# Optimization experiments

Hardware: AMD Instinct MI355X
Metric: run time of the kernel (lower is better)

## Reference

```python
import jax, jax.numpy as jnp
import numpy as np
import math

N_HEADS = 16

def _ln(x, g, b, eps=1e-5):
    m = jnp.mean(x, axis=-1, keepdims=True)
    v = jnp.var(x, axis=-1, keepdims=True)
    return (x - m) * jax.lax.rsqrt(v + eps) * g + b

def _block(x, ln1_g, ln1_b, ln2_g, ln2_b, wqkv, wo, w1, w2):
    b, k, d = x.shape
    dh = d // N_HEADS
    h = _ln(x, ln1_g, ln1_b)
    qkv = (h @ wqkv).reshape(b, k, 3, N_HEADS, dh)
    q, kk, v = qkv[:, :, 0], qkv[:, :, 1], qkv[:, :, 2]
    scores = jnp.einsum('bqhd,bkhd->bhqk', q, kk) / math.sqrt(dh)
    attn = jax.nn.softmax(scores, axis=-1)
    o = jnp.einsum('bhqk,bkhd->bqhd', attn, v).reshape(b, k, d) @ wo
    x = x + o
    h2 = _ln(x, ln2_g, ln2_b)
    return x + jax.nn.gelu(h2 @ w1) @ w2

def setup_inputs() -> dict:
    key = jax.random.key(0)
    ks = jax.random.split(key, 6)
    b, s, d, dff = 4, 4096, 1024, 4096
    sc = 0.02
    return {
        'x': jax.random.normal(ks[0], (b, s, d), jnp.float32),
        'router_w': jax.random.normal(ks[1], (d,), jnp.float32) * sc,
        'ln1_g': jnp.ones((d,), jnp.float32),
        'ln1_b': jnp.zeros((d,), jnp.float32),
        'ln2_g': jnp.ones((d,), jnp.float32),
        'ln2_b': jnp.zeros((d,), jnp.float32),
        'wqkv': jax.random.normal(ks[2], (d, 3 * d), jnp.float32) * sc,
        'wo': jax.random.normal(ks[3], (d, d), jnp.float32) * sc,
        'w1': jax.random.normal(ks[4], (d, dff), jnp.float32) * sc,
        'w2': jax.random.normal(ks[5], (dff, d), jnp.float32) * sc,
    }

def reference(x, router_w, ln1_g, ln1_b, ln2_g, ln2_b, wqkv, wo, w1, w2):
    b, s, d = x.shape
    K = s // 2  # top_k = int(s * capacity_factor), capacity_factor = 0.5
    logits = x @ router_w                      # [b, s]
    w, idx = jax.lax.top_k(logits, K)          # [b, K]
    order = jnp.argsort(idx, axis=1)           # sort selected tokens by position
    sel = jnp.take_along_axis(idx, order, axis=1)          # [b, K] sorted indices
    fx = jnp.take_along_axis(x, sel[..., None], axis=1)    # gather routed tokens [b, K, d]
    xo = _block(fx, ln1_g, ln1_b, ln2_g, ln2_b, wqkv, wo, w1, w2)
    rw = jnp.take_along_axis(jax.nn.softmax(w, axis=1), order, axis=1)[..., None]  # [b, K, 1]
    batch_idx = jnp.arange(b)[:, None]
    out = x.at[batch_idx, sel].add(rw * xo)    # softmax-weighted scatter-add
    return out
```

## Files before the change

### kernel.cpp

```cpp
#include <hip/hip_runtime.h>
#include <hip/hip_bf16.h>
#include <stdint.h>

typedef __hip_bfloat16 bf16;
typedef __attribute__((ext_vector_type(8))) short short8;
typedef __attribute__((ext_vector_type(4))) float f32x4;
typedef __attribute__((ext_vector_type(2))) unsigned uint2v;
typedef __attribute__((ext_vector_type(4))) unsigned uint4v;
typedef __attribute__((ext_vector_type(4))) unsigned short ushort4v;

#define B_   4
#define S_   4096
#define D_   1024
#define KSEL 2048
#define DFF  4096
#define NH   16
#define DH   64

static __device__ __forceinline__ void load_lds16(const void* g, void* l) {
  __builtin_amdgcn_global_load_lds((const __attribute__((address_space(1))) void*)g,
                                   (__attribute__((address_space(3))) void*)l,
                                   16, 0, 0);
}

static __device__ __forceinline__ short8 scale8(short8 v, float s) {
  short8 r;
#pragma unroll
  for (int i = 0; i < 8; ++i) {
    unsigned u = ((unsigned)(unsigned short)v[i]) << 16;
    float f = __uint_as_float(u) * s;
    bf16 o = __float2bfloat16(f);
    short t;
    __builtin_memcpy(&t, &o, 2);
    r[i] = t;
  }
  return r;
}

static __device__ __forceinline__ unsigned cvt_pk_bf16(float lo, float hi) {
  unsigned r;
  asm("v_cvt_pk_bf16_f32 %0, %1, %2" : "=v"(r) : "v"(lo), "v"(hi));
  return r;
}

static __device__ __forceinline__ void pl32_swap(unsigned &a, unsigned &b) {
#if __has_builtin(__builtin_amdgcn_permlane32_swap)
  uint2v r = __builtin_amdgcn_permlane32_swap(a, b, false, false);
  a = r[0]; b = r[1];
#else
  asm("v_permlane32_swap_b32 %0, %1" : "+v"(a), "+v"(b));
#endif
}

static __device__ __forceinline__ void pl16_swap(unsigned &a, unsigned &b) {
#if __has_builtin(__builtin_amdgcn_permlane16_swap)
  uint2v r = __builtin_amdgcn_permlane16_swap(a, b, false, false);
  a = r[0]; b = r[1];
#else
  asm("v_permlane16_swap_b32 %0, %1" : "+v"(a), "+v"(b));
#endif
}

__global__ __launch_bounds__(256)
void copy_router(const float* __restrict__ x, const float* __restrict__ rwts,
                 float* __restrict__ out, float* __restrict__ logits)
{
  int s = blockIdx.x, b = blockIdx.y;
  int tid = threadIdx.x;
  const float4* row = (const float4*)(x + ((size_t)b * S_ + s) * D_);
  float4 v = row[tid];
  ((float4*)(out + ((size_t)b * S_ + s) * D_))[tid] = v;
  float4 rv = ((const float4*)rwts)[tid];
  float p = v.x * rv.x + v.y * rv.y + v.z * rv.z + v.w * rv.w;
  for (int off = 32; off; off >>= 1) p += __shfl_down(p, off, 64);
  __shared__ float wsum[4];
  if ((tid & 63) == 0) wsum[tid >> 6] = p;
  __syncthreads();
  if (tid == 0) logits[(size_t)b * S_ + s] = wsum[0] + wsum[1] + wsum[2] + wsum[3];
}

__global__ __launch_bounds__(1024)
void topk_kernel(const float* __restrict__ logits,
                 int* __restrict__ sel, float* __restrict__ rw)
{
  __shared__ float lg[4096];
  __shared__ unsigned long long keys[4096];
  __shared__ unsigned char flags[4096];
  __shared__ float wsum[16];
  __shared__ int wtot[16];
  __shared__ int woff[17];

  int b = blockIdx.x, tid = threadIdx.x;
  const float* L = logits + (size_t)b * S_;
  for (int i = tid; i < 4096; i += 1024) {
    float v = L[i];
    lg[i] = v;
    unsigned u = __float_as_uint(v);
    u = (u & 0x80000000u) ? ~u : (u | 0x80000000u);
    u = ~u;
    keys[i] = ((unsigned long long)u << 32) | (unsigned)i;
  }
  __syncthreads();
  for (int k = 2; k <= 4096; k <<= 1) {
    for (int j = k >> 1; j > 0; j >>= 1) {
      for (int t = tid; t < 4096; t += 1024) {
        int ixj = t ^ j;
        if (ixj > t) {
          bool up = ((t & k) == 0);
          unsigned long long a = keys[t], c = keys[ixj];
          if ((a > c) == up) { keys[t] = c; keys[ixj] = a; }
        }
      }
      __syncthreads();
    }
  }
  for (int i = tid; i < 4096; i += 1024) flags[i] = 0;
  __syncthreads();
  for (int i = tid; i < KSEL; i += 1024) flags[(int)(keys[i] & 0xFFFFFFFFu)] = 1;
  __syncthreads();
  float m = lg[(int)(keys[0] & 0xFFFFFFFFu)];
  float part = 0.f;
  for (int i = tid; i < KSEL; i += 1024) part += __expf(lg[(int)(keys[i] & 0xFFFFFFFFu)] - m);
  for (int off = 32; off; off >>= 1) part += __shfl_down(part, off, 64);
  if ((tid & 63) == 0) wsum[tid >> 6] = part;
  __syncthreads();
  if (tid == 0) { float t = 0; for (int w = 0; w < 16; ++w) t += wsum[w]; wsum[0] = t; }
  __syncthreads();
  float inv = 1.0f / wsum[0];
  int base = tid * 4;
  int f0 = flags[base], f1 = flags[base + 1], f2 = flags[base + 2], f3 = flags[base + 3];
  int mysum = f0 + f1 + f2 + f3;
  int incl = mysum;
  int lane = tid & 63;
  for (int off = 1; off < 64; off <<= 1) {
    int t = __shfl_up(incl, off, 64);
    if (lane >= off) incl += t;
  }
  if (lane == 63) wtot[tid >> 6] = incl;
  __syncthreads();
  if (tid == 0) { int sacc = 0; for (int w = 0; w < 16; ++w) { woff[w] = sacc; sacc += wtot[w]; } woff[16] = sacc; }
  __syncthreads();
  int p = woff[tid >> 6] + incl - mysum;
  int fl[4] = { f0, f1, f2, f3 };
  for (int q = 0; q < 4; ++q) {
    if (fl[q]) {
      int idx = base + q;
      sel[b * KSEL + p] = idx;
      rw[b * KSEL + p] = __expf(lg[idx] - m) * inv;
      p++;
    }
  }
}

__global__ __launch_bounds__(256)
void ln_kernel(const float* __restrict__ in, const float* __restrict__ x,
               const int* __restrict__ sel,
               const float* __restrict__ g, const float* __restrict__ beta,
               bf16* __restrict__ out, int gather)
{
  int r = blockIdx.x;
  int tid = threadIdx.x;
  const float* src;
  if (gather) {
    int b = r >> 11, t = r & 2047;
    src = x + ((size_t)b * S_ + sel[b * KSEL + t]) * D_;
  } else {
    src = in + (size_t)r * D_;
  }
  float4 v = ((const float4*)src)[tid];
  float s = v.x + v.y + v.z + v.w;
  float sq = v.x * v.x + v.y * v.y + v.z * v.z + v.w * v.w;
  for (int off = 32; off; off >>= 1) { s += __shfl_down(s, off, 64); sq += __shfl_down(sq, off, 64); }
  __shared__ float wsA[4], wsB[4];
  if ((tid & 63) == 0) { wsA[tid >> 6] = s; wsB[tid >> 6] = sq; }
  __syncthreads();
  float stot = wsA[0] + wsA[1] + wsA[2] + wsA[3];
  float sqt  = wsB[0] + wsB[1] + wsB[2] + wsB[3];
  float mean = stot * (1.f / 1024.f);
  float var  = sqt * (1.f / 1024.f) - mean * mean;
  float rs = rsqrtf(var + 1e-5f);
  float4 gv = ((const float4*)g)[tid];
  float4 bv = ((const float4*)beta)[tid];
  bf16* o = out + (size_t)r * D_ + tid * 4;
  o[0] = __float2bfloat16((v.x - mean) * rs * gv.x + bv.x);
  o[1] = __float2bfloat16((v.y - mean) * rs * gv.y + bv.y);
  o[2] = __float2bfloat16((v.z - mean) * rs * gv.z + bv.z);
  o[3] = __float2bfloat16((v.w - mean) * rs * gv.w + bv.w);
}

__global__ __launch_bounds__(256)
void wtrans(const float* __restrict__ in, bf16* __restrict__ out, int K, int N)
{
  __shared__ float tile[32][33];
  int n0 = blockIdx.x * 32, k0 = blockIdx.y * 32;
  int r = threadIdx.x >> 5, c = threadIdx.x & 31;
#pragma unroll
  for (int i = 0; i < 4; ++i)
    tile[r + 8 * i][c] = in[(size_t)(k0 + r + 8 * i) * N + n0 + c];
  __syncthreads();
#pragma unroll
  for (int i = 0; i < 4; ++i)
    out[(size_t)(n0 + r + 8 * i) * K + k0 + c] = __float2bfloat16(tile[c][r + 8 * i]);
}

__global__ __launch_bounds__(256)
void vt_transpose(const bf16* __restrict__ qkv, bf16* __restrict__ vt)
{
  __shared__ bf16 tile[32][33];
  int bh = blockIdx.z;
  int d0 = blockIdx.y * 32;
  int t0 = blockIdx.x * 32;
  int b = bh >> 4, h = bh & 15;
  int r = threadIdx.x >> 5, c = threadIdx.x & 31;
#pragma unroll
  for (int i = 0; i < 4; ++i) {
    int t = t0 + r + 8 * i;
    tile[r + 8 * i][c] = qkv[(size_t)(b * KSEL + t) * 3072 + 2048 + h * 64 + d0 + c];
  }
  __syncthreads();
#pragma unroll
  for (int i = 0; i < 4; ++i) {
    int d = d0 + r + 8 * i;
    vt[((size_t)bh * 64 + d) * KSEL + t0 + c] = tile[c][r + 8 * i];
  }
}

template<int EPI, int TN>
__global__ __launch_bounds__(256)
void gemm_bt(const bf16* __restrict__ A, const bf16* __restrict__ Bt,
             float* __restrict__ Cf, bf16* __restrict__ Cb,
             int M, int N, int K,
             const float* __restrict__ xin, const int* __restrict__ sel,
             const float* __restrict__ rw, const float* __restrict__ x1,
             float* __restrict__ outp)
{
  constexpr int NT = TN / 32;
  constexpr int WN = TN / 2;
  __shared__ bf16 As[128 * 64];
  __shared__ bf16 Bs[TN * 64];
  const int tid = threadIdx.x;
  const int wid = tid >> 6;
  const int lane = tid & 63;
  const int l15 = lane & 15;
  const int quad = lane >> 4;
  const int wm = wid >> 1, wn = wid & 1;
  const int bm = blockIdx.x * 128;
  const int bn = blockIdx.y * TN;

  const int srow = lane >> 3;
  const int sgrp = (lane & 7) ^ srow;

  f32x4 acc[4][NT] = {};

  for (int k0 = 0; k0 < K; k0 += 64) {
#pragma unroll
    for (int c2 = 0; c2 < 4; ++c2) {
      int c = wid * 4 + c2;
      const bf16* ga = A + (size_t)(bm + c * 8 + srow) * K + (k0 + sgrp * 8);
      load_lds16(ga, &As[c * 512]);
    }
#pragma unroll
    for (int c2 = 0; c2 < TN / 32; ++c2) {
      int c = wid * (TN / 32) + c2;
      const bf16* gb = Bt + (size_t)(bn + c * 8 + srow) * K + (k0 + sgrp * 8);
      load_lds16(gb, &Bs[c * 512]);
    }
    __syncthreads();
#pragma unroll
    for (int ks = 0; ks < 2; ++ks) {
      short8 af[4], bfv[NT];
#pragma unroll
      for (int mt = 0; mt < 4; ++mt) {
        int row = wm * 64 + mt * 16 + l15;
        int cg = (ks * 4 + quad) ^ (row & 7);
        af[mt] = *(const short8*)&As[row * 64 + cg * 8];
      }
#pragma unroll
      for (int nt = 0; nt < NT; ++nt) {
        int row = wn * WN + nt * 16 + l15;
        int cg = (ks * 4 + quad) ^ (row & 7);
        bfv[nt] = *(const short8*)&Bs[row * 64 + cg * 8];
      }
#pragma unroll
      for (int mt = 0; mt < 4; ++mt)
#pragma unroll
        for (int nt = 0; nt < NT; ++nt)
          acc[mt][nt] = __builtin_amdgcn_mfma_f32_16x16x32_bf16(af[mt], bfv[nt], acc[mt][nt], 0, 0, 0);
    }
    __syncthreads();
  }

#pragma unroll
  for (int mt = 0; mt < 4; ++mt) {
#pragma unroll
    for (int r = 0; r < 4; ++r) {
      int gm = bm + wm * 64 + mt * 16 + quad * 4 + r;
      int bb = gm >> 11, tt = gm & 2047;
      int sr = 0; float rwv = 0.f;
      if (EPI == 1 || EPI == 3) sr = sel[bb * KSEL + tt];
      if (EPI == 3) rwv = rw[bb * KSEL + tt];
#pragma unroll
      for (int nt = 0; nt < NT; ++nt) {
        int gn = bn + wn * WN + nt * 16 + l15;
        float v = acc[mt][nt][r];
        if (EPI == 0) {
          Cb[(size_t)gm * N + gn] = __float2bfloat16(v);
        } else if (EPI == 1) {
          float xv = xin[((size_t)bb * S_ + sr) * D_ + gn];
          Cf[(size_t)gm * N + gn] = xv + v;
        } else if (EPI == 2) {
          float u = v;
          float cc = 0.7978845608028654f * (u + 0.044715f * u * u * u);
          float e = __expf(2.f * cc);
          float th = 1.f - 2.f / (e + 1.f);
          Cb[(size_t)gm * N + gn] = __float2bfloat16(0.5f * u * (1.f + th));
        } else {
          float v2 = rwv * (x1[(size_t)gm * D_ + gn] + v);
          outp[((size_t)bb * S_ + sr) * D_ + gn] += v2;
        }
      }
    }
  }
}

__global__ __launch_bounds__(256)
void flash_kernel(const bf16* __restrict__ qkv, const bf16* __restrict__ vt,
                  bf16* __restrict__ attn_o)
{
  __shared__ bf16 Ks[128 * 64];
  __shared__ bf16 Vs[64 * 128];
  int qt = blockIdx.x, h = blockIdx.y, b = blockIdx.z;
  int tid = threadIdx.x, wid = tid >> 6, lane = tid & 63;
  int l15 = lane & 15, quad = lane >> 4;
  int q0 = qt * 128 + wid * 32;

  const int srowK = lane >> 3, sgK = lane & 7;
  const int srowV = lane >> 4, sgV = lane & 15;

  short8 qf[2][2];
#pragma unroll
  for (int mt = 0; mt < 2; ++mt)
#pragma unroll
    for (int ks = 0; ks < 2; ++ks) {
      const bf16* p = qkv + (size_t)(b * KSEL + q0 + mt * 16 + l15) * 3072 + h * 64 + ks * 32 + quad * 8;
      qf[mt][ks] = scale8(*(const short8*)p, 0.125f * 1.44269504f);
    }

  f32x4 acc_ot[2][4] = {};
  float lsum[2] = {};

  const bf16* Vg = vt + (size_t)(b * NH + h) * 64 * KSEL;

  for (int kt = 0; kt < KSEL / 128; ++kt) {
    int tok0 = b * KSEL + kt * 128;
    __syncthreads();
#pragma unroll
    for (int i = 0; i < 4; ++i) {
      int c = wid * 4 + i;
      const bf16* ga = qkv + (size_t)(tok0 + c * 8 + srowK) * 3072 + 1024 + h * 64 + ((sgK ^ srowK) * 8);
      load_lds16(ga, &Ks[c * 512]);
      int vr = c * 4 + srowV;
      const bf16* gv = Vg + (size_t)vr * KSEL + kt * 128 + ((sgV ^ (vr & 7)) * 8);
      load_lds16(gv, &Vs[c * 512]);
    }
    __syncthreads();

#pragma unroll
    for (int ks4 = 0; ks4 < 4; ++ks4) {
      f32x4 s[2][2] = {};
#pragma unroll
      for (int u = 0; u < 2; ++u) {
        int row = (ks4 * 2 + u) * 16 + l15;
#pragma unroll
        for (int ks = 0; ks < 2; ++ks) {
          int g = (ks * 4 + quad) ^ (row & 7);
          short8 kf = *(const short8*)&Ks[row * 64 + g * 8];
#pragma unroll
          for (int mt = 0; mt < 2; ++mt)
            s[mt][u] = __builtin_amdgcn_mfma_f32_16x16x32_bf16(kf, qf[mt][ks], s[mt][u], 0, 0, 0);
        }
      }
      short8 pfrag[2];
#pragma unroll
      for (int mt = 0; mt < 2; ++mt) {
        float pA[4], pB[4];
#pragma unroll
        for (int r = 0; r < 4; ++r) {
          pA[r] = __builtin_amdgcn_exp2f(s[mt][0][r]);
          pB[r] = __builtin_amdgcn_exp2f(s[mt][1][r]);
          lsum[mt] += pA[r] + pB[r];
        }
        unsigned A0 = cvt_pk_bf16(pA[0], pA[1]);
        unsigned A1 = cvt_pk_bf16(pA[2], pA[3]);
        unsigned B0 = cvt_pk_bf16(pB[0], pB[1]);
        unsigned B1 = cvt_pk_bf16(pB[2], pB[3]);
        pl32_swap(A0, B0); pl16_swap(A0, B0);
        pl32_swap(A1, B1); pl16_swap(A1, B1);
        uint4v w; w[0] = A0; w[1] = A1; w[2] = B0; w[3] = B1;
        pfrag[mt] = __builtin_bit_cast(short8, w);
      }
#pragma unroll
      for (int dt = 0; dt < 4; ++dt) {
        int row = dt * 16 + l15;
        int g = (ks4 * 4 + quad) ^ (row & 7);
        short8 vf = *(const short8*)&Vs[row * 128 + g * 8];
#pragma unroll
        for (int mt = 0; mt < 2; ++mt)
          acc_ot[mt][dt] = __builtin_amdgcn_mfma_f32_16x16x32_bf16(vf, pfrag[mt], acc_ot[mt][dt], 0, 0, 0);
      }
    }
  }
#pragma unroll
  for (int mt = 0; mt < 2; ++mt) {
    float l = lsum[mt];
    l += __shfl_xor(l, 16, 64);
    l += __shfl_xor(l, 32, 64);
    float invl = 1.0f / l;
#pragma unroll
    for (int dt = 0; dt < 4; ++dt) {
      ushort4v o;
#pragma unroll
      for (int r = 0; r < 4; ++r) {
        bf16 t = __float2bfloat16(acc_ot[mt][dt][r] * invl);
        unsigned short us;
        __builtin_memcpy(&us, &t, 2);
        o[r] = us;
      }
      *(ushort4v*)(attn_o + (size_t)(b * KSEL + q0 + mt * 16 + l15) * D_ + h * 64 + dt * 16 + quad * 4) = o;
    }
  }
}

extern "C" void kernel_launch(void* const* d_in, const int* in_sizes, int n_in,
                              void* d_out, int out_size, void* d_ws, size_t ws_size,
                              hipStream_t stream)
{
  const float* x      = (const float*)d_in[0];
  const float* router = (const float*)d_in[1];
  const float* ln1g   = (const float*)d_in[2];
  const float* ln1b   = (const float*)d_in[3];
  const float* ln2g   = (const float*)d_in[4];
  const float* ln2b   = (const float*)d_in[5];
  const float* wqkv   = (const float*)d_in[6];
  const float* wo     = (const float*)d_in[7];
  const float* w1     = (const float*)d_in[8];
  const float* w2     = (const float*)d_in[9];
  float* out = (float*)d_out;
  char* ws = (char*)d_ws;

  float* logits = (float*)(ws + 0);
  int*   sel    = (int*)  (ws + 65536);
  float* rw     = (float*)(ws + 98304);
  bf16* wqkvT   = (bf16*) (ws + 131072);
  bf16* woT     = (bf16*) (ws + 6422528);
  bf16* w1T     = (bf16*) (ws + 8519680);
  bf16* w2T     = (bf16*) (ws + 16908288);
  bf16* regA    = (bf16*) (ws + 25296896);
  bf16* regB    = (bf16*) (ws + 42074112);
  bf16* vtb     = (bf16*) (ws + 42074112 + 50331648);
  float* x1     = (float*)(ws + 109182976);

  copy_router<<<dim3(S_, B_), 256, 0, stream>>>(x, router, out, logits);
  topk_kernel<<<B_, 1024, 0, stream>>>(logits, sel, rw);

  wtrans<<<dim3(3072 / 32, 1024 / 32), 256, 0, stream>>>(wqkv, wqkvT, 1024, 3072);
  wtrans<<<dim3(1024 / 32, 1024 / 32), 256, 0, stream>>>(wo,   woT,   1024, 1024);
  wtrans<<<dim3(4096 / 32, 1024 / 32), 256, 0, stream>>>(w1,   w1T,   1024, 4096);
  wtrans<<<dim3(1024 / 32, 4096 / 32), 256, 0, stream>>>(w2,   w2T,   4096, 1024);

  ln_kernel<<<B_ * KSEL, 256, 0, stream>>>(nullptr, x, sel, ln1g, ln1b, regA, 1);

  gemm_bt<0, 128><<<dim3(64, 24), 256, 0, stream>>>(regA, wqkvT, nullptr, regB, 8192, 3072, 1024,
                                                    nullptr, nullptr, nullptr, nullptr, nullptr);
  vt_transpose<<<dim3(KSEL / 32, 2, B_ * NH), 256, 0, stream>>>(regB, vtb);
  flash_kernel<<<dim3(KSEL / 128, NH, B_), 256, 0, stream>>>(regB, vtb, regA);

  gemm_bt<1, 64><<<dim3(64, 16), 256, 0, stream>>>(regA, woT, x1, nullptr, 8192, 1024, 1024,
                                                   x, sel, nullptr, nullptr, nullptr);
  ln_kernel<<<B_ * KSEL, 256, 0, stream>>>(x1, nullptr, nullptr, ln2g, ln2b, regA, 0);
  gemm_bt<2, 128><<<dim3(64, 32), 256, 0, stream>>>(regA, w1T, nullptr, regB, 8192, 4096, 1024,
                                                    nullptr, nullptr, nullptr, nullptr, nullptr);
  gemm_bt<3, 64><<<dim3(64, 16), 256, 0, stream>>>(regB, w2T, nullptr, nullptr, 8192, 1024, 4096,
                                                   nullptr, sel, rw, x1, out);
}
```

Baseline: 645.7 us.

## Add 256x256 pipelined GEMM kernel for QKV and FFN1 projections

Adds a new 512-thread GEMM kernel with 256x256 output tiles and swizzled LDS layout. It double-buffers tiles through direct global-to-LDS loads, interleaving staging with MFMA phases using explicit vmcnt waits, barriers and setprio. The kernel is used for the QKV and W1+GELU projections to raise data reuse and overlap memory with compute. The wo and w2 GEMMs are also switched to 128-wide N tiles. Risks are fewer blocks (384/512) against the CU count, higher register pressure with 2 blocks per CU, and fragile hand-written wait counts.

Result: no change. 640.5 us (-0.8%).

```diff
diff --git a/kernel.cpp b/kernel.cpp
--- a/kernel.cpp
+++ b/kernel.cpp
@@ -59,6 +59,15 @@
 #else
   asm("v_permlane16_swap_b32 %0, %1" : "+v"(a), "+v"(b));
 #endif
+}
+
+static __device__ __forceinline__ void wait_vm6() {
+  asm volatile("s_waitcnt vmcnt(6)" ::: "memory");
+  __builtin_amdgcn_sched_barrier(0);
+}
+static __device__ __forceinline__ void wait_vm0() {
+  asm volatile("s_waitcnt vmcnt(0)" ::: "memory");
+  __builtin_amdgcn_sched_barrier(0);
 }
 
 __global__ __launch_bounds__(256)
@@ -225,6 +234,120 @@
   }
 }
 
+#define STA(TILE, KH)                                                           \
+  do { int kc_ = (TILE) * 64 + (KH) * 32 + kp;                                  \
+    load_lds16(A + (size_t)(bm + sr0) * K + kc_, &lds[(TILE) & 1][0][KH][wid * 1024]);        \
+    load_lds16(A + (size_t)(bm + sr1) * K + kc_, &lds[(TILE) & 1][0][KH][wid * 1024 + 512]);  \
+  } while (0)
+#define STB(TILE, KH)                                                           \
+  do { int kc_ = (TILE) * 64 + (KH) * 32 + kp;                                  \
+    load_lds16(Bt + (size_t)(bn + sr0) * K + kc_, &lds[(TILE) & 1][1][KH][wid * 1024]);       \
+    load_lds16(Bt + (size_t)(bn + sr1) * K + kc_, &lds[(TILE) & 1][1][KH][wid * 1024 + 512]); \
+  } while (0)
+
+#define GPH(BSEL, KH, NG, STAGE_STMT, WAIT_STMT)                                \
+  do {                                                                          \
+    if (NG == 0) {                                                              \
+      _Pragma("unroll")                                                         \
+      for (int mt = 0; mt < 8; ++mt) {                                          \
+        int r_ = wm * 128 + mt * 16 + l15;                                      \
+        int R_ = r_ >> 1;                                                       \
+        int gp_ = (((r_ & 1) << 2) + quad) ^ (R_ & 7);                          \
+        af[mt] = *(const short8*)&lds[BSEL][0][KH][R_ * 64 + gp_ * 8];          \
+      }                                                                         \
+    }                                                                           \
+    short8 bfr0, bfr1;                                                          \
+    {                                                                           \
+      int rb_ = wn * 64 + (NG * 2) * 16 + l15;                                  \
+      int Rb_ = rb_ >> 1;                                                       \
+      int gpb_ = (((rb_ & 1) << 2) + quad) ^ (Rb_ & 7);                         \
+      bfr0 = *(const short8*)&lds[BSEL][1][KH][Rb_ * 64 + gpb_ * 8];            \
+      int rc_ = rb_ + 16;                                                       \
+      int Rc_ = rc_ >> 1;                                                       \
+      int gpc_ = (((rc_ & 1) << 2) + quad) ^ (Rc_ & 7);                         \
+      bfr1 = *(const short8*)&lds[BSEL][1][KH][Rc_ * 64 + gpc_ * 8];            \
+    }                                                                           \
+    STAGE_STMT;                                                                 \
+    __builtin_amdgcn_s_barrier();                                               \
+    asm volatile("s_waitcnt lgkmcnt(0)" ::: "memory");                          \
+    __builtin_amdgcn_sched_barrier(0);                                          \
+    __builtin_amdgcn_s_setprio(1);                                              \
+    _Pragma("unroll")                                                           \
+    for (int mt = 0; mt < 8; ++mt) {                                            \
+      acc[mt][NG * 2]     = __builtin_amdgcn_mfma_f32_16x16x32_bf16(af[mt], bfr0, acc[mt][NG * 2], 0, 0, 0);     \
+      acc[mt][NG * 2 + 1] = __builtin_amdgcn_mfma_f32_16x16x32_bf16(af[mt], bfr1, acc[mt][NG * 2 + 1], 0, 0, 0); \
+    }                                                                           \
+    __builtin_amdgcn_s_setprio(0);                                              \
+    WAIT_STMT;                                                                  \
+    __builtin_amdgcn_s_barrier();                                               \
+  } while (0)
+
+template<int EPI>
+__global__ __launch_bounds__(512, 2)
+void gemm256(const bf16* __restrict__ A, const bf16* __restrict__ Bt,
+             bf16* __restrict__ Cb, int M, int N, int K)
+{
+  __shared__ bf16 lds[2][2][2][128 * 64];
+  const int tid = threadIdx.x;
+  const int wid = tid >> 6;
+  const int lane = tid & 63;
+  const int l15 = lane & 15;
+  const int quad = lane >> 4;
+  const int wm = wid >> 2, wn = wid & 3;
+  const int bm = blockIdx.x * 256;
+  const int bn = blockIdx.y * 256;
+
+  const int sgv = (lane & 7) ^ (lane >> 3);
+  const int sr0 = wid * 32 + (lane >> 3) * 2 + (sgv >> 2);
+  const int sr1 = sr0 + 16;
+  const int kp  = (sgv & 3) * 8;
+
+  f32x4 acc[8][4] = {};
+  short8 af[8];
+
+  const int NI = K >> 7;
+
+  STA(0, 0); STB(0, 0); STA(0, 1); STB(0, 1);
+  STA(1, 0); STB(1, 0); STA(1, 1);
+  wait_vm6();
+  __builtin_amdgcn_s_barrier();
+
+  for (int J = 0; J < NI; ++J) {
+    const bool more = (J < NI - 1);
+    const int t2 = 2 * J + 2, t3 = 2 * J + 3;
+    GPH(0, 0, 0, STB(2 * J + 1, 1), ((void)0));
+    GPH(0, 0, 1, if (more) STA(t2, 0), ((void)0));
+    GPH(0, 1, 0, if (more) STB(t2, 0), ((void)0));
+    GPH(0, 1, 1, if (more) STA(t2, 1), if (more) wait_vm6(); else wait_vm0());
+    GPH(1, 0, 0, if (more) STB(t2, 1), ((void)0));
+    GPH(1, 0, 1, if (more) STA(t3, 0), ((void)0));
+    GPH(1, 1, 0, if (more) STB(t3, 0), ((void)0));
+    GPH(1, 1, 1, if (more) STA(t3, 1), if (more) wait_vm6());
+  }
+
+#pragma unroll
+  for (int mt = 0; mt < 8; ++mt) {
+#pragma unroll
+    for (int r = 0; r < 4; ++r) {
+      int gm = bm + wm * 128 + mt * 16 + quad * 4 + r;
+#pragma unroll
+      for (int nt = 0; nt < 4; ++nt) {
+        int gn = bn + wn * 64 + nt * 16 + l15;
+        float v = acc[mt][nt][r];
+        if (EPI == 0) {
+          Cb[(size_t)gm * N + gn] = __float2bfloat16(v);
+        } else {
+          float u = v;
+          float cc = 0.7978845608028654f * (u + 0.044715f * u * u * u);
+          float e = __expf(2.f * cc);
+          float th = 1.f - 2.f / (e + 1.f);
+          Cb[(size_t)gm * N + gn] = __float2bfloat16(0.5f * u * (1.f + th));
+        }
+      }
+    }
+  }
+}
+
 template<int EPI, int TN>
 __global__ __launch_bounds__(256)
 void gemm_bt(const bf16* __restrict__ A, const bf16* __restrict__ Bt,
@@ -303,17 +426,9 @@
       for (int nt = 0; nt < NT; ++nt) {
         int gn = bn + wn * WN + nt * 16 + l15;
         float v = acc[mt][nt][r];
-        if (EPI == 0) {
-          Cb[(size_t)gm * N + gn] = __float2bfloat16(v);
-        } else if (EPI == 1) {
+        if (EPI == 1) {
           float xv = xin[((size_t)bb * S_ + sr) * D_ + gn];
           Cf[(size_t)gm * N + gn] = xv + v;
-        } else if (EPI == 2) {
-          float u = v;
-          float cc = 0.7978845608028654f * (u + 0.044715f * u * u * u);
-          float e = __expf(2.f * cc);
-          float th = 1.f - 2.f / (e + 1.f);
-          Cb[(size_t)gm * N + gn] = __float2bfloat16(0.5f * u * (1.f + th));
         } else {
           float v2 = rwv * (x1[(size_t)gm * D_ + gn] + v);
           outp[((size_t)bb * S_ + sr) * D_ + gn] += v2;
@@ -470,16 +585,14 @@
 
   ln_kernel<<<B_ * KSEL, 256, 0, stream>>>(nullptr, x, sel, ln1g, ln1b, regA, 1);
 
-  gemm_bt<0, 128><<<dim3(64, 24), 256, 0, stream>>>(regA, wqkvT, nullptr, regB, 8192, 3072, 1024,
-                                                    nullptr, nullptr, nullptr, nullptr, nullptr);
+  gemm256<0><<<dim3(32, 12), 512, 0, stream>>>(regA, wqkvT, regB, 8192, 3072, 1024);
   vt_transpose<<<dim3(KSEL / 32, 2, B_ * NH), 256, 0, stream>>>(regB, vtb);
   flash_kernel<<<dim3(KSEL / 128, NH, B_), 256, 0, stream>>>(regB, vtb, regA);
 
-  gemm_bt<1, 64><<<dim3(64, 16), 256, 0, stream>>>(regA, woT, x1, nullptr, 8192, 1024, 1024,
+  gemm_bt<1, 128><<<dim3(64, 8), 256, 0, stream>>>(regA, woT, x1, nullptr, 8192, 1024, 1024,
                                                    x, sel, nullptr, nullptr, nullptr);
   ln_kernel<<<B_ * KSEL, 256, 0, stream>>>(x1, nullptr, nullptr, ln2g, ln2b, regA, 0);
-  gemm_bt<2, 128><<<dim3(64, 32), 256, 0, stream>>>(regA, w1T, nullptr, regB, 8192, 4096, 1024,
-                                                    nullptr, nullptr, nullptr, nullptr, nullptr);
-  gemm_bt<3, 64><<<dim3(64, 16), 256, 0, stream>>>(regB, w2T, nullptr, nullptr, 8192, 1024, 4096,
+  gemm256<2><<<dim3(32, 16), 512, 0, stream>>>(regA, w1T, regB, 8192, 4096, 1024);
+  gemm_bt<3, 128><<<dim3(64, 8), 256, 0, stream>>>(regB, w2T, nullptr, nullptr, 8192, 1024, 4096,
                                                    nullptr, sel, rw, x1, out);
 }
```
